# Kernel tuning notes

Measured on AMD Instinct MI355X. Metric: run time of the kernel, lower is better.

Reference implementation:

```python
import jax, jax.numpy as jnp
from jax import lax
import numpy as np

N, C, T, V = 128, 64, 128, 25   # batch, channels, frames, joints
S, R, O, K = 3, 8, 64, 5        # subsets, rel_channels, out_channels, temporal kernel
BC, AC = 16, 16                 # branch channels, attention channels
EPS = 1e-5


def _bn(x, g, b):
    # eval-mode BatchNorm2d with running_mean=0, running_var=1
    return x * (g / jnp.sqrt(1.0 + EPS))[None, :, None, None] + b[None, :, None, None]


def _c1x1(x, w, b):
    # 1x1 conv over channel dim; x [N,C,T,V], w [O,C], b [O]
    return jnp.einsum('oc,nctv->notv', w, x) + b[None, :, None, None]


def _tconv(x, w, b, d):
    # temporal conv, kernel (K,1), dilation (d,1), 'same' padding in T; w [O,I,K]
    pad = (K + (K - 1) * (d - 1) - 1) // 2
    out = lax.conv_general_dilated(x, w[..., None], (1, 1), [(pad, pad), (0, 0)],
                                   rhs_dilation=(d, 1),
                                   dimension_numbers=('NCHW', 'OIHW', 'NCHW'))
    return out + b[None, :, None, None]


def setup_inputs() -> dict:
    ks = iter(jax.random.split(jax.random.key(0), 40))
    nrm = lambda sh, s=0.1: jax.random.normal(next(ks), sh, jnp.float32) * s
    z = lambda sh: jnp.zeros(sh, jnp.float32)
    o = lambda sh: jnp.ones(sh, jnp.float32)
    return {
        'x': jax.random.normal(next(ks), (N, C, T, V), jnp.float32),
        'PA': nrm((S, V, V)),
        'alpha': o((S,)),
        'c1w': nrm((S, R, C)), 'c1b': z((S, R)),
        'c2w': nrm((S, R, C)), 'c2b': z((S, R)),
        'c3w': nrm((S, O, C)), 'c3b': z((S, O)),
        'c4w': nrm((S, O, R)), 'c4b': z((S, O)),
        'gbn_g': o((O,)), 'gbn_b': z((O,)),
        'att1_w': nrm((AC, O)), 'att1_b': z((AC,)),
        'att2_w': nrm((O, AC)), 'att2_b': z((O,)),
        'br_pw': nrm((2, BC, O)), 'br_pb': z((2, BC)),
        'br_pg': o((2, BC)), 'br_pbeta': z((2, BC)),
        'br_tw': nrm((2, BC, BC, K)), 'br_tb': z((2, BC)),
        'br_tg': o((2, BC)), 'br_tbeta': z((2, BC)),
        'mp_pw': nrm((BC, O)), 'mp_pb': z((BC,)),
        'mp_g1': o((BC,)), 'mp_b1': z((BC,)),
        'mp_g2': o((BC,)), 'mp_b2': z((BC,)),
        'p3w': nrm((BC, O)), 'p3b': z((BC,)),
        'p3g': o((BC,)), 'p3beta': z((BC,)),
    }


def reference(x, PA, alpha, c1w, c1b, c2w, c2b, c3w, c3b, c4w, c4b,
              gbn_g, gbn_b, att1_w, att1_b, att2_w, att2_b,
              br_pw, br_pb, br_pg, br_pbeta, br_tw, br_tb, br_tg, br_tbeta,
              mp_pw, mp_pb, mp_g1, mp_b1, mp_g2, mp_b2, p3w, p3b, p3g, p3beta):
    # ---- unit_ctrgcn: 3 CTRGC subsets vectorized over axis s ----
    xm = x.mean(axis=2)                                       # [N,C,V]; 1x1 conv commutes with mean over T
    x1 = jnp.einsum('src,ncv->nsrv', c1w, xm) + c1b[None, :, :, None]
    x2 = jnp.einsum('src,ncv->nsrv', c2w, xm) + c2b[None, :, :, None]
    x3 = jnp.einsum('soc,nctv->nsotv', c3w, x) + c3b[None, :, :, None, None]
    diff = jnp.tanh(x1[..., :, None] - x2[..., None, :])      # [N,S,R,U,V]
    aff = jnp.einsum('sor,nsruv->nsouv', c4w, diff) + c4b[None, :, :, None, None]
    Asym = PA + jnp.swapaxes(PA, -1, -2)                      # A + A^T, [S,V,V]
    aff = aff * alpha[None, :, None, None, None] + Asym[None, :, None, :, :]
    aff = jax.nn.softmax(aff, axis=-2)                        # softmax over u (dim=-2)
    y = jnp.einsum('nsouv,nsotv->notu', aff, x3)              # aggregate + sum over subsets
    y = _bn(y, gbn_g, gbn_b)
    # squeeze-excite channel attention
    pooled = y.mean(axis=(2, 3))                              # [N,O]
    h = jax.nn.relu(pooled @ att1_w.T + att1_b)
    se = jax.nn.sigmoid(h @ att2_w.T + att2_b)
    y = jax.nn.relu(y * se[:, :, None, None] + x)             # down = identity (in==out, stride 1)
    # ---- MultiScale_TemporalConv (residual=False), stride 1 ----
    outs = []
    for i, d in enumerate((1, 2)):
        p = jax.nn.relu(_bn(_c1x1(y, br_pw[i], br_pb[i]), br_pg[i], br_pbeta[i]))
        t = _tconv(p, br_tw[i], br_tb[i], d)
        outs.append(_bn(t, br_tg[i], br_tbeta[i]))
    p = jax.nn.relu(_bn(_c1x1(y, mp_pw, mp_pb), mp_g1, mp_b1))
    m = lax.reduce_window(p, -jnp.inf, lax.max, (1, 1, 3, 1), (1, 1, 1, 1),
                          [(0, 0), (0, 0), (1, 1), (0, 0)])   # MaxPool2d((3,1), stride 1, pad (1,0))
    outs.append(_bn(m, mp_g2, mp_b2))
    outs.append(_bn(_c1x1(y, p3w, p3b), p3g, p3beta))
    out = jnp.concatenate(outs, axis=1)
    return jax.nn.relu(out + x)                               # outer residual (identity) + relu
```

## Files before the change

kernel.cpp:

```cpp
#include <hip/hip_runtime.h>
#include <hip/hip_bf16.h>
#include <math.h>

#define N_  128
#define C_  64
#define T_  128
#define V_  25
#define S_  3
#define R_  8
#define O_  64
#define BC_ 16
#define TV_ 3200

typedef __attribute__((ext_vector_type(8))) short bf16x8;
typedef __attribute__((ext_vector_type(4))) float f32x4;

__device__ inline short f2bf(float f) {
  union { float f; unsigned u; } c; c.f = f;
  unsigned r = (c.u + 0x7FFFu + ((c.u >> 16) & 1u)) >> 16;
  return (short)r;
}
__device__ inline float bf2f(short s) {
  union { float f; unsigned u; } c; c.u = ((unsigned)(unsigned short)s) << 16;
  return c.f;
}

__global__ __launch_bounds__(256) void k_cvt(const float* __restrict__ x,
                                             const float* __restrict__ c3w,
                                             const float* __restrict__ br_tw,
                                             short* __restrict__ xbfT,
                                             short* __restrict__ c3wbf,
                                             short* __restrict__ w2g) {
  int bid = blockIdx.x;
  int tid = threadIdx.x;
  if (bid < 6400) {
    int n = bid / 50, pg = bid % 50;
    int w = tid >> 6, l = tid & 63;
    int p0 = pg * 64 + w * 16;
    const float* xp = x + ((size_t)n * 64 + l) * TV_ + p0;
    short* ob = xbfT + ((size_t)n * TV_ + p0) * 64 + l;
    #pragma unroll
    for (int q = 0; q < 4; ++q) {
      float4 xv = *(const float4*)(xp + q * 4);
      ob[(q * 4 + 0) * 64] = f2bf(xv.x);
      ob[(q * 4 + 1) * 64] = f2bf(xv.y);
      ob[(q * 4 + 2) * 64] = f2bf(xv.z);
      ob[(q * 4 + 3) * 64] = f2bf(xv.w);
    }
    if (bid < 144) {
      int i = bid * 256 + tid;
      c3wbf[i] = f2bf(c3w[i]);
    }
  } else {
    for (int i = tid; i < 6144; i += 256) {
      int plane = i / 3072, rem = i % 3072;
      int h = rem / 1536, rem2 = rem % 1536;
      int bc = rem2 / 96, kidx = rem2 % 96;
      short outv = 0;
      if (kidx < 80) {
        int ktap = kidx >> 4, ic = kidx & 15;
        float wv = br_tw[((h * 16 + bc) * 16 + ic) * 5 + ktap];
        short wb = f2bf(wv);
        outv = (plane == 0) ? wb : f2bf(wv - bf2f(wb));
      }
      w2g[i] = outv;
    }
  }
}

__global__ __launch_bounds__(256) void k_xm(const float* __restrict__ x,
                                            float* __restrict__ xm) {
  int nc = blockIdx.x;
  const float* xp = x + (size_t)nc * TV_;
  __shared__ float part[250];
  int tid = threadIdx.x;
  if (tid < 250) {
    float s = 0.f;
    for (int k = 0; k < 13; ++k) {
      int idx = tid + 250 * k;
      if (idx < TV_) s += xp[idx];
    }
    part[tid] = s;
  }
  __syncthreads();
  if (tid < 25) {
    float s = 0.f;
    #pragma unroll
    for (int g = 0; g < 10; ++g) s += part[g * 25 + tid];
    xm[(size_t)nc * V_ + tid] = s * (1.0f / 128.0f);
  }
}

__global__ __launch_bounds__(256) void k_aff(
    const float* __restrict__ xm, const float* __restrict__ PA,
    const float* __restrict__ alpha,
    const float* __restrict__ c1w, const float* __restrict__ c1b,
    const float* __restrict__ c2w, const float* __restrict__ c2b,
    const float* __restrict__ c4w, const float* __restrict__ c4b,
    short* __restrict__ affbf) {
  int oq = blockIdx.x, s = blockIdx.y, n = blockIdx.z;
  int tid = threadIdx.x;
  __shared__ float xml[1600];
  __shared__ float w1[512], w2[512], w4l[512];
  __shared__ float x1l[200], x2l[200];
  __shared__ float dift[625 * 9];
  __shared__ float asym[625];
  short* ab = affbf + (((size_t)n * S_ + s) * 64) * 1024;
  {
    int4 zz; zz.x = 0; zz.y = 0; zz.z = 0; zz.w = 0;
    int4* z0 = (int4*)(ab + (size_t)(oq * 8) * 1024);
    int4* z1 = (int4*)(ab + (size_t)(oq * 8 + 32) * 1024);
    for (int i = tid; i < 1024; i += 256) { z0[i] = zz; z1[i] = zz; }
  }
  for (int i = tid; i < 1600; i += 256) xml[i] = xm[(size_t)n * 1600 + i];
  for (int i = tid; i < 512; i += 256) {
    w1[i] = c1w[s * 512 + i];
    w2[i] = c2w[s * 512 + i];
    w4l[i] = c4w[s * 512 + i];
  }
  for (int i = tid; i < 625; i += 256) {
    int u = i / 25, v = i % 25;
    asym[i] = PA[s * 625 + u * 25 + v] + PA[s * 625 + v * 25 + u];
  }
  __syncthreads();
  if (tid < 200) {
    int r = tid / 25, v = tid % 25;
    float a1 = c1b[s * R_ + r], a2 = c2b[s * R_ + r];
    #pragma unroll
    for (int c = 0; c < 64; ++c) {
      float xv = xml[c * 25 + v];
      a1 = fmaf(w1[r * 64 + c], xv, a1);
      a2 = fmaf(w2[r * 64 + c], xv, a2);
    }
    x1l[tid] = a1; x2l[tid] = a2;
  }
  __syncthreads();
  for (int i = tid; i < 5000; i += 256) {
    int r = i / 625, rem = i % 625, u = rem / 25, v = rem % 25;
    dift[(u * 25 + v) * 9 + r] = tanhf(x1l[r * 25 + u] - x2l[r * 25 + v]);
  }
  __syncthreads();
  float al = alpha[s];
  if (tid < 200) {
    int ol = tid / 25, v = tid % 25;
    int oA = oq * 8 + ol, oB = oA + 32;
    float avA[25], avB[25];
    float bA = c4b[s * O_ + oA], bB = c4b[s * O_ + oB];
    #pragma unroll
    for (int u = 0; u < 25; ++u) { avA[u] = bA; avB[u] = bB; }
    #pragma unroll
    for (int u = 0; u < 25; ++u) {
      const float* dp = &dift[(u * 25 + v) * 9];
      #pragma unroll
      for (int r = 0; r < 8; ++r) {
        float d = dp[r];
        avA[u] = fmaf(w4l[oA * 8 + r], d, avA[u]);
        avB[u] = fmaf(w4l[oB * 8 + r], d, avB[u]);
      }
    }
    float mA = -1e30f, mB = -1e30f;
    #pragma unroll
    for (int u = 0; u < 25; ++u) {
      float as_ = asym[u * 25 + v];
      avA[u] = fmaf(avA[u], al, as_);
      avB[u] = fmaf(avB[u], al, as_);
      mA = fmaxf(mA, avA[u]); mB = fmaxf(mB, avB[u]);
    }
    float sA = 0.f, sB = 0.f;
    #pragma unroll
    for (int u = 0; u < 25; ++u) {
      avA[u] = expf(avA[u] - mA); sA += avA[u];
      avB[u] = expf(avB[u] - mB); sB += avB[u];
    }
    float iA = 1.0f / sA, iB = 1.0f / sB;
    #pragma unroll
    for (int u = 0; u < 25; ++u) {
      ab[(size_t)oA * 1024 + u * 32 + v] = f2bf(avA[u] * iA);
      ab[(size_t)oB * 1024 + u * 32 + v] = f2bf(avB[u] * iB);
    }
  }
}

__global__ __launch_bounds__(256) void k_gemm1(
    const short* __restrict__ xbfT, const short* __restrict__ c3wbf,
    const float* __restrict__ c3b, short* __restrict__ x3p, int n0) {
  int pt = blockIdx.x;
  int nn = blockIdx.y;
  int n = n0 + nn;
  int tid = threadIdx.x, w = tid >> 6, l = tid & 63;
  int lr = l & 15, lg = l >> 4;
  const short* xb = xbfT + ((size_t)n * TV_ + pt * 64) * 64;
  bf16x8 B[4][2];
  #pragma unroll
  for (int sub = 0; sub < 4; ++sub) {
    const short* rp = xb + (sub * 16 + lr) * 64 + lg * 8;
    B[sub][0] = *(const bf16x8*)(rp);
    B[sub][1] = *(const bf16x8*)(rp + 32);
  }
  bf16x8 A[3][2];
  #pragma unroll
  for (int m = 0; m < 3; ++m) {
    const short* rp = c3wbf + (size_t)((w * 3 + m) * 16 + lr) * 64 + lg * 8;
    A[m][0] = *(const bf16x8*)(rp);
    A[m][1] = *(const bf16x8*)(rp + 32);
  }
  f32x4 acc[3][4];
  #pragma unroll
  for (int m = 0; m < 3; ++m)
    #pragma unroll
    for (int sub = 0; sub < 4; ++sub) acc[m][sub] = (f32x4)(0.f);
  #pragma unroll
  for (int m = 0; m < 3; ++m)
    #pragma unroll
    for (int sub = 0; sub < 4; ++sub) {
      acc[m][sub] = __builtin_amdgcn_mfma_f32_16x16x32_bf16(A[m][0], B[sub][0], acc[m][sub], 0, 0, 0);
      acc[m][sub] = __builtin_amdgcn_mfma_f32_16x16x32_bf16(A[m][1], B[sub][1], acc[m][sub], 0, 0, 0);
    }
  int tl[4], vl[4];
  #pragma unroll
  for (int sub = 0; sub < 4; ++sub) {
    int pos = pt * 64 + sub * 16 + lr;
    tl[sub] = pos / 25; vl[sub] = pos - tl[sub] * 25;
  }
  #pragma unroll
  for (int m = 0; m < 3; ++m) {
    int mt = w * 3 + m;
    #pragma unroll
    for (int j = 0; j < 4; ++j) {
      int r = mt * 16 + lg * 4 + j;
      float bias = c3b[r];
      short* orow = x3p + (((size_t)nn * 192 + r) * 128) * 32;
      #pragma unroll
      for (int sub = 0; sub < 4; ++sub) {
        orow[tl[sub] * 32 + vl[sub]] = f2bf(acc[m][sub][j] + bias);
      }
    }
  }
}

__global__ __launch_bounds__(256) void k_gemm2(
    const short* __restrict__ x3p, const short* __restrict__ affbf,
    const float* __restrict__ gbn_g, const float* __restrict__ gbn_b,
    short* __restrict__ ybn, float* __restrict__ pooled, int n0) {
  int og = blockIdx.x;
  int nn = blockIdx.y;
  int n = n0 + nn;
  int tid = threadIdx.x, w = tid >> 6, l = tid & 63;
  int lr = l & 15, lg = l >> 4;
  int o = og * 4 + w;
  f32x4 acc[8][2];
  #pragma unroll
  for (int mt = 0; mt < 8; ++mt) { acc[mt][0] = (f32x4)(0.f); acc[mt][1] = (f32x4)(0.f); }
  const short* xb = x3p + (((size_t)nn * 3) * 64 + o) * 4096;
  const short* ab = affbf + (((size_t)n * 3) * 64 + o) * 1024;
  #pragma unroll
  for (int s = 0; s < 3; ++s) {
    const short* abs_ = ab + (size_t)s * 64 * 1024;
    bf16x8 Bf[2];
    Bf[0] = *(const bf16x8*)(abs_ + (0 * 16 + lr) * 32 + lg * 8);
    Bf[1] = *(const bf16x8*)(abs_ + (1 * 16 + lr) * 32 + lg * 8);
    const short* xbs = xb + (size_t)s * 64 * 4096;
    #pragma unroll
    for (int mt = 0; mt < 8; ++mt) {
      bf16x8 Af = *(const bf16x8*)(xbs + (mt * 16 + lr) * 32 + lg * 8);
      acc[mt][0] = __builtin_amdgcn_mfma_f32_16x16x32_bf16(Af, Bf[0], acc[mt][0], 0, 0, 0);
      acc[mt][1] = __builtin_amdgcn_mfma_f32_16x16x32_bf16(Af, Bf[1], acc[mt][1], 0, 0, 0);
    }
  }
  float rs = 1.0f / sqrtf(1.0f + 1e-5f);
  float sc = gbn_g[o] * rs, bb = gbn_b[o];
  short* yb = ybn + ((size_t)n * 64 + o) * TV_;
  float lsum = 0.f;
  #pragma unroll
  for (int mt = 0; mt < 8; ++mt) {
    #pragma unroll
    for (int j = 0; j < 4; ++j) {
      int t = mt * 16 + lg * 4 + j;
      float v0 = fmaf(acc[mt][0][j], sc, bb);
      yb[t * 25 + lr] = f2bf(v0); lsum += v0;
      if (lr < 9) {
        float v1 = fmaf(acc[mt][1][j], sc, bb);
        yb[t * 25 + 16 + lr] = f2bf(v1); lsum += v1;
      }
    }
  }
  #pragma unroll
  for (int off = 32; off > 0; off >>= 1) lsum += __shfl_down(lsum, off);
  if (l == 0) pooled[(size_t)n * 64 + o] = lsum;
}

__global__ __launch_bounds__(64) void k_se(
    const float* __restrict__ pooled,
    const float* __restrict__ att1_w, const float* __restrict__ att1_b,
    const float* __restrict__ att2_w, const float* __restrict__ att2_b,
    float* __restrict__ se) {
  int n = blockIdx.x; int tid = threadIdx.x;
  __shared__ float pl[64]; __shared__ float hbuf[16];
  pl[tid] = pooled[(size_t)n * 64 + tid] * (1.0f / 3200.0f);
  __syncthreads();
  if (tid < 16) {
    float a = att1_b[tid];
    #pragma unroll
    for (int o = 0; o < 64; ++o) a = fmaf(att1_w[tid * 64 + o], pl[o], a);
    hbuf[tid] = fmaxf(a, 0.f);
  }
  __syncthreads();
  float a2 = att2_b[tid];
  #pragma unroll
  for (int k = 0; k < 16; ++k) a2 = fmaf(att2_w[tid * 16 + k], hbuf[k], a2);
  se[(size_t)n * 64 + tid] = 1.0f / (1.0f + expf(-a2));
}

__global__ __launch_bounds__(256) void k_pw(
    const short* __restrict__ ybn, const float* __restrict__ se,
    const float* __restrict__ x,
    const float* __restrict__ br_pw, const float* __restrict__ br_pb,
    const float* __restrict__ br_pg, const float* __restrict__ br_pbeta,
    const float* __restrict__ mp_pw, const float* __restrict__ mp_pb,
    const float* __restrict__ mp_g1, const float* __restrict__ mp_b1,
    const float* __restrict__ p3w, const float* __restrict__ p3b,
    const float* __restrict__ p3g, const float* __restrict__ p3beta,
    short* __restrict__ pbuf, float* __restrict__ outp) {
  int tt = blockIdx.x; int n = blockIdx.y;
  int t0 = tt * 10;
  int npos = min(10, T_ - t0) * 25;
  int tid = threadIdx.x;
  if (tid >= npos) return;
  float rs = 1.0f / sqrtf(1.0f + 1e-5f);
  size_t base = (size_t)n * C_ * TV_ + (size_t)t0 * 25 + tid;
  int pos = t0 * 25 + tid;
  const float* sep = se + (size_t)n * 64;
  float y2[64]; float xhi[16];
  #pragma unroll
  for (int o = 0; o < 64; ++o) {
    float xv = x[base + (size_t)o * TV_];
    float yv = bf2f(ybn[base + (size_t)o * TV_]);
    y2[o] = fmaxf(fmaf(yv, sep[o], xv), 0.f);
    if (o >= 48) xhi[o - 48] = xv;
  }
  #pragma unroll
  for (int h = 0; h < 3; ++h) {
    const float* wp = (h == 0) ? br_pw : (h == 1) ? (br_pw + 1024) : mp_pw;
    short* po = pbuf + ((size_t)(h * N_ + n) * TV_ + pos) * 16;
    bf16x8 v0, v1;
    #pragma unroll
    for (int bc = 0; bc < 16; ++bc) {
      float g, beta, pb;
      if (h < 2) { g = br_pg[h * 16 + bc]; beta = br_pbeta[h * 16 + bc]; pb = br_pb[h * 16 + bc]; }
      else       { g = mp_g1[bc];          beta = mp_b1[bc];             pb = mp_pb[bc]; }
      float a = 0.f;
      #pragma unroll
      for (int o = 0; o < 64; ++o) a = fmaf(wp[bc * 64 + o], y2[o], a);
      short pk = f2bf(fmaxf(fmaf(a + pb, g * rs, beta), 0.f));
      if (bc < 8) v0[bc] = pk; else v1[bc - 8] = pk;
    }
    *(bf16x8*)(po) = v0;
    *(bf16x8*)(po + 8) = v1;
  }
  #pragma unroll
  for (int bc = 0; bc < 16; ++bc) {
    float a = 0.f;
    #pragma unroll
    for (int o = 0; o < 64; ++o) a = fmaf(p3w[bc * 64 + o], y2[o], a);
    float ov = fmaf(a + p3b[bc], p3g[bc] * rs, p3beta[bc]);
    outp[base + (size_t)(48 + bc) * TV_] = fmaxf(ov + xhi[bc], 0.f);
  }
}

__global__ __launch_bounds__(256) void k_tcm(
    const short* __restrict__ pbuf, const short* __restrict__ w2g,
    const float* __restrict__ x,
    const float* __restrict__ br_tb, const float* __restrict__ br_tg,
    const float* __restrict__ br_tbeta,
    float* __restrict__ outp) {
  int tt = blockIdx.x, h = blockIdx.y, n = blockIdx.z;
  int d = 1 + h;
  int tid = threadIdx.x, w = tid >> 6, l = tid & 63;
  int lr = l & 15, lg = l >> 4;
  __shared__ short ptile[72 * 25 * 16];
  {
    const int4* src = (const int4*)(pbuf + ((size_t)(h * N_ + n) * TV_) * 16);
    int4* dst = (int4*)ptile;
    int4 zz; zz.x = 0; zz.y = 0; zz.z = 0; zz.w = 0;
    for (int u = tid; u < 3600; u += 256) {
      int r = u / 50, q = u - r * 50;
      int t = tt * 64 - 4 + r;
      dst[u] = (t >= 0 && t < T_) ? src[t * 50 + q] : zz;
    }
  }
  bf16x8 Af0[3], Af1[3];
  #pragma unroll
  for (int ks = 0; ks < 3; ++ks) {
    Af0[ks] = *(const bf16x8*)(w2g + ((0 * 2 + h) * 16 + lr) * 96 + ks * 32 + lg * 8);
    Af1[ks] = *(const bf16x8*)(w2g + ((1 * 2 + h) * 16 + lr) * 96 + ks * 32 + lg * 8);
  }
  float rs = 1.0f / sqrtf(1.0f + 1e-5f);
  float scl[4], shf[4];
  #pragma unroll
  for (int j = 0; j < 4; ++j) {
    int bc = lg * 4 + j;
    float sc = br_tg[h * 16 + bc] * rs;
    scl[j] = sc;
    shf[j] = fmaf(br_tb[h * 16 + bc], sc, br_tbeta[h * 16 + bc]);
  }
  __syncthreads();
  for (int nt = w; nt < 100; nt += 4) {
    int posL = nt * 16 + lr;
    int tL = posL / 25, v = posL - tL * 25;
    f32x4 acc = (f32x4)(0.f);
    #pragma unroll
    for (int ks = 0; ks < 3; ++ks) {
      int ktap = 2 * ks + (lg >> 1);
      int ic0 = (lg & 1) * 8;
      int r = tL + 4 + (ktap - 2) * d;
      r = min(r, 71);
      bf16x8 Bf = *(const bf16x8*)(ptile + (r * 25 + v) * 16 + ic0);
      acc = __builtin_amdgcn_mfma_f32_16x16x32_bf16(Af0[ks], Bf, acc, 0, 0, 0);
      acc = __builtin_amdgcn_mfma_f32_16x16x32_bf16(Af1[ks], Bf, acc, 0, 0, 0);
    }
    int gpos = tt * 1600 + posL;
    #pragma unroll
    for (int j = 0; j < 4; ++j) {
      int ch = h * 16 + lg * 4 + j;
      size_t oa = ((size_t)n * 64 + ch) * TV_ + gpos;
      float xv = x[oa];
      outp[oa] = fmaxf(fmaf(acc[j], scl[j], shf[j]) + xv, 0.f);
    }
  }
}

__global__ __launch_bounds__(256) void k_mp(
    const short* __restrict__ pbuf, const float* __restrict__ x,
    const float* __restrict__ mp_g2, const float* __restrict__ mp_b2,
    float* __restrict__ outp) {
  int tt = blockIdx.x, n = blockIdx.y;
  int t0 = tt * 10;
  int npos = min(10, T_ - t0) * 25;
  int tid = threadIdx.x;
  if (tid >= npos) return;
  int pos = t0 * 25 + tid;
  int t = pos / 25, v = pos - t * 25;
  const short* pb = pbuf + ((size_t)(2 * N_ + n) * TV_) * 16;
  int tm = max(t - 1, 0), tp = min(t + 1, T_ - 1);
  bf16x8 a0 = *(const bf16x8*)(pb + (tm * 25 + v) * 16);
  bf16x8 a1 = *(const bf16x8*)(pb + (tm * 25 + v) * 16 + 8);
  bf16x8 b0 = *(const bf16x8*)(pb + (t  * 25 + v) * 16);
  bf16x8 b1 = *(const bf16x8*)(pb + (t  * 25 + v) * 16 + 8);
  bf16x8 c0 = *(const bf16x8*)(pb + (tp * 25 + v) * 16);
  bf16x8 c1 = *(const bf16x8*)(pb + (tp * 25 + v) * 16 + 8);
  float rs = 1.0f / sqrtf(1.0f + 1e-5f);
  #pragma unroll
  for (int i = 0; i < 8; ++i) {
    float m0 = fmaxf(fmaxf(bf2f(a0[i]), bf2f(b0[i])), bf2f(c0[i]));
    float m1 = fmaxf(fmaxf(bf2f(a1[i]), bf2f(b1[i])), bf2f(c1[i]));
    size_t oa0 = ((size_t)n * 64 + 32 + i) * TV_ + pos;
    size_t oa1 = ((size_t)n * 64 + 40 + i) * TV_ + pos;
    float v0 = fmaf(m0, mp_g2[i] * rs, mp_b2[i]);
    float v1 = fmaf(m1, mp_g2[8 + i] * rs, mp_b2[8 + i]);
    outp[oa0] = fmaxf(v0 + x[oa0], 0.f);
    outp[oa1] = fmaxf(v1 + x[oa1], 0.f);
  }
}

extern "C" void kernel_launch(void* const* d_in, const int* in_sizes, int n_in,
                              void* d_out, int out_size, void* d_ws, size_t ws_size,
                              hipStream_t stream) {
  (void)in_sizes; (void)n_in; (void)out_size; (void)ws_size;
  const float* x      = (const float*)d_in[0];
  const float* PA     = (const float*)d_in[1];
  const float* alpha  = (const float*)d_in[2];
  const float* c1w    = (const float*)d_in[3];
  const float* c1b    = (const float*)d_in[4];
  const float* c2w    = (const float*)d_in[5];
  const float* c2b    = (const float*)d_in[6];
  const float* c3w    = (const float*)d_in[7];
  const float* c3b    = (const float*)d_in[8];
  const float* c4w    = (const float*)d_in[9];
  const float* c4b    = (const float*)d_in[10];
  const float* gbn_g  = (const float*)d_in[11];
  const float* gbn_b  = (const float*)d_in[12];
  const float* att1_w = (const float*)d_in[13];
  const float* att1_b = (const float*)d_in[14];
  const float* att2_w = (const float*)d_in[15];
  const float* att2_b = (const float*)d_in[16];
  const float* br_pw  = (const float*)d_in[17];
  const float* br_pb  = (const float*)d_in[18];
  const float* br_pg  = (const float*)d_in[19];
  const float* br_pbeta = (const float*)d_in[20];
  const float* br_tw  = (const float*)d_in[21];
  const float* br_tb  = (const float*)d_in[22];
  const float* br_tg  = (const float*)d_in[23];
  const float* br_tbeta = (const float*)d_in[24];
  const float* mp_pw  = (const float*)d_in[25];
  const float* mp_pb  = (const float*)d_in[26];
  const float* mp_g1  = (const float*)d_in[27];
  const float* mp_b1  = (const float*)d_in[28];
  const float* mp_g2  = (const float*)d_in[29];
  const float* mp_b2  = (const float*)d_in[30];
  const float* p3w    = (const float*)d_in[31];
  const float* p3b    = (const float*)d_in[32];
  const float* p3g    = (const float*)d_in[33];
  const float* p3beta = (const float*)d_in[34];
  float* out = (float*)d_out;
  float* ws  = (float*)d_ws;

  float* xm_b    = ws;
  float* pooled  = ws + 204800;
  float* se_b    = ws + 212992;
  short* xbfT    = (short*)(ws + 221184);
  short* affbf   = (short*)(ws + 13328384);
  short* x3p     = (short*)(ws + 25911296);
  short* ybn     = (short*)(ws + 38494208);
  short* c3wbf   = (short*)(ws + 51601408);
  short* w2g     = (short*)(ws + 51619840);
  short* p_b     = (short*)(ws + 13328384);

  k_cvt<<<dim3(6401),        dim3(256), 0, stream>>>(x, c3w, br_tw, xbfT, c3wbf, w2g);
  k_xm <<<dim3(N_ * C_),     dim3(256), 0, stream>>>(x, xm_b);
  k_aff<<<dim3(4, 3, N_),    dim3(256), 0, stream>>>(xm_b, PA, alpha, c1w, c1b, c2w, c2b,
                                                     c4w, c4b, affbf);
  for (int ch = 0; ch < 4; ++ch) {
    k_gemm1<<<dim3(50, 32), dim3(256), 0, stream>>>(xbfT, c3wbf, c3b, x3p, ch * 32);
    k_gemm2<<<dim3(16, 32), dim3(256), 0, stream>>>(x3p, affbf, gbn_g, gbn_b, ybn, pooled, ch * 32);
  }
  k_se <<<dim3(N_),          dim3(64),  0, stream>>>(pooled, att1_w, att1_b, att2_w, att2_b, se_b);
  k_pw <<<dim3(13, N_),      dim3(256), 0, stream>>>(ybn, se_b, x, br_pw, br_pb, br_pg, br_pbeta,
                                                     mp_pw, mp_pb, mp_g1, mp_b1,
                                                     p3w, p3b, p3g, p3beta, p_b, out);
  k_tcm<<<dim3(2, 2, N_),    dim3(256), 0, stream>>>(p_b, w2g, x, br_tb, br_tg, br_tbeta, out);
  k_mp <<<dim3(13, N_),      dim3(256), 0, stream>>>(p_b, x, mp_g2, mp_b2, out);
}
```

Measured before the change: 671.3 us.

## Move pointwise branch convolutions onto MFMA with split-bf16 weights and folded BN

Replaces the scalar-FMA pointwise kernel, which held 64 y2 values per thread, with an MFMA kernel. Each block stages a 128-position tile of y2 as hi/lo bf16 pairs in swizzled LDS, and each wave computes one 16-channel branch through three bf16 MFMAs to approximate fp32 accuracy. BN scale and bias are folded into precomputed split-bf16 weights and a shift vector inside the conversion kernel. This removes heavy per-thread FMA work and register pressure, at the cost of extra LDS traffic and a small approximation error.

```diff
diff --git a/kernel.cpp b/kernel.cpp
--- a/kernel.cpp
+++ b/kernel.cpp
@@ -28,11 +28,26 @@
 __global__ __launch_bounds__(256) void k_cvt(const float* __restrict__ x,
                                              const float* __restrict__ c3w,
                                              const float* __restrict__ br_tw,
+                                             const float* __restrict__ br_pw,
+                                             const float* __restrict__ br_pb,
+                                             const float* __restrict__ br_pg,
+                                             const float* __restrict__ br_pbeta,
+                                             const float* __restrict__ mp_pw,
+                                             const float* __restrict__ mp_pb,
+                                             const float* __restrict__ mp_g1,
+                                             const float* __restrict__ mp_b1,
+                                             const float* __restrict__ p3w,
+                                             const float* __restrict__ p3b,
+                                             const float* __restrict__ p3g,
+                                             const float* __restrict__ p3beta,
                                              short* __restrict__ xbfT,
                                              short* __restrict__ c3wbf,
-                                             short* __restrict__ w2g) {
+                                             short* __restrict__ w2g,
+                                             short* __restrict__ wcbf,
+                                             float* __restrict__ wcsh) {
   int bid = blockIdx.x;
   int tid = threadIdx.x;
+  float rs = 1.0f / sqrtf(1.0f + 1e-5f);
   if (bid < 6400) {
     int n = bid / 50, pg = bid % 50;
     int w = tid >> 6, l = tid & 63;
@@ -64,6 +79,27 @@
         outv = (plane == 0) ? wb : f2bf(wv - bf2f(wb));
       }
       w2g[i] = outv;
+    }
+    for (int i = tid; i < 4096; i += 256) {
+      int r = i / 64, c = i % 64;
+      int br = r >> 4, bc = r & 15;
+      float wv, g;
+      if (br < 2)      { wv = br_pw[br * 1024 + bc * 64 + c]; g = br_pg[br * 16 + bc]; }
+      else if (br == 2){ wv = mp_pw[bc * 64 + c];             g = mp_g1[bc]; }
+      else             { wv = p3w[bc * 64 + c];               g = p3g[bc]; }
+      float ws_ = wv * (g * rs);
+      short hi = f2bf(ws_);
+      wcbf[i] = hi;
+      wcbf[4096 + i] = f2bf(ws_ - bf2f(hi));
+    }
+    if (tid < 64) {
+      int r = tid;
+      int br = r >> 4, bc = r & 15;
+      float g, pb, beta;
+      if (br < 2)      { g = br_pg[br * 16 + bc]; pb = br_pb[br * 16 + bc]; beta = br_pbeta[br * 16 + bc]; }
+      else if (br == 2){ g = mp_g1[bc];           pb = mp_pb[bc];           beta = mp_b1[bc]; }
+      else             { g = p3g[bc];             pb = p3b[bc];             beta = p3beta[bc]; }
+      wcsh[r] = fmaf(pb, g * rs, beta);
     }
   }
 }
@@ -311,59 +347,84 @@
   se[(size_t)n * 64 + tid] = 1.0f / (1.0f + expf(-a2));
 }
 
-__global__ __launch_bounds__(256) void k_pw(
+__global__ __launch_bounds__(256) void k_pwm(
     const short* __restrict__ ybn, const float* __restrict__ se,
     const float* __restrict__ x,
-    const float* __restrict__ br_pw, const float* __restrict__ br_pb,
-    const float* __restrict__ br_pg, const float* __restrict__ br_pbeta,
-    const float* __restrict__ mp_pw, const float* __restrict__ mp_pb,
-    const float* __restrict__ mp_g1, const float* __restrict__ mp_b1,
-    const float* __restrict__ p3w, const float* __restrict__ p3b,
-    const float* __restrict__ p3g, const float* __restrict__ p3beta,
+    const short* __restrict__ wcbf, const float* __restrict__ wcsh,
     short* __restrict__ pbuf, float* __restrict__ outp) {
-  int tt = blockIdx.x; int n = blockIdx.y;
-  int t0 = tt * 10;
-  int npos = min(10, T_ - t0) * 25;
+  int pt = blockIdx.x; int n = blockIdx.y;
   int tid = threadIdx.x;
-  if (tid >= npos) return;
-  float rs = 1.0f / sqrtf(1.0f + 1e-5f);
-  size_t base = (size_t)n * C_ * TV_ + (size_t)t0 * 25 + tid;
-  int pos = t0 * 25 + tid;
-  const float* sep = se + (size_t)n * 64;
-  float y2[64]; float xhi[16];
-  #pragma unroll
-  for (int o = 0; o < 64; ++o) {
-    float xv = x[base + (size_t)o * TV_];
-    float yv = bf2f(ybn[base + (size_t)o * TV_]);
-    y2[o] = fmaxf(fmaf(yv, sep[o], xv), 0.f);
-    if (o >= 48) xhi[o - 48] = xv;
-  }
-  #pragma unroll
-  for (int h = 0; h < 3; ++h) {
-    const float* wp = (h == 0) ? br_pw : (h == 1) ? (br_pw + 1024) : mp_pw;
-    short* po = pbuf + ((size_t)(h * N_ + n) * TV_ + pos) * 16;
-    bf16x8 v0, v1;
-    #pragma unroll
-    for (int bc = 0; bc < 16; ++bc) {
-      float g, beta, pb;
-      if (h < 2) { g = br_pg[h * 16 + bc]; beta = br_pbeta[h * 16 + bc]; pb = br_pb[h * 16 + bc]; }
-      else       { g = mp_g1[bc];          beta = mp_b1[bc];             pb = mp_pb[bc]; }
-      float a = 0.f;
+  __shared__ short yl[2][128 * 64];
+  {
+    int posL = tid & 127, ch = tid >> 7;
+    int pos0 = pt * 128;
+    const float* sep = se + (size_t)n * 64;
+    float y2r[32];
+    #pragma unroll
+    for (int i = 0; i < 32; ++i) {
+      int c = ch * 32 + i;
+      size_t a = ((size_t)n * 64 + c) * TV_ + pos0 + posL;
+      float xv = x[a];
+      float yv = bf2f(ybn[a]);
+      y2r[i] = fmaxf(fmaf(yv, sep[c], xv), 0.f);
+    }
+    #pragma unroll
+    for (int q = 0; q < 4; ++q) {
+      bf16x8 hi, lo;
       #pragma unroll
-      for (int o = 0; o < 64; ++o) a = fmaf(wp[bc * 64 + o], y2[o], a);
-      short pk = f2bf(fmaxf(fmaf(a + pb, g * rs, beta), 0.f));
-      if (bc < 8) v0[bc] = pk; else v1[bc - 8] = pk;
-    }
-    *(bf16x8*)(po) = v0;
-    *(bf16x8*)(po + 8) = v1;
-  }
-  #pragma unroll
-  for (int bc = 0; bc < 16; ++bc) {
-    float a = 0.f;
-    #pragma unroll
-    for (int o = 0; o < 64; ++o) a = fmaf(p3w[bc * 64 + o], y2[o], a);
-    float ov = fmaf(a + p3b[bc], p3g[bc] * rs, p3beta[bc]);
-    outp[base + (size_t)(48 + bc) * TV_] = fmaxf(ov + xhi[bc], 0.f);
+      for (int j = 0; j < 8; ++j) {
+        float v = y2r[q * 8 + j];
+        short hb = f2bf(v);
+        hi[j] = hb;
+        lo[j] = f2bf(v - bf2f(hb));
+      }
+      int cc = ch * 4 + q;
+      int ccs = cc ^ (posL & 7);
+      *(bf16x8*)&yl[0][posL * 64 + ccs * 8] = hi;
+      *(bf16x8*)&yl[1][posL * 64 + ccs * 8] = lo;
+    }
+  }
+  __syncthreads();
+  int w = tid >> 6, l = tid & 63;
+  int lr = l & 15, lg = l >> 4;
+  bf16x8 A0[2], A1[2];
+  #pragma unroll
+  for (int kk = 0; kk < 2; ++kk) {
+    A0[kk] = *(const bf16x8*)(wcbf +        (w * 16 + lr) * 64 + kk * 32 + lg * 8);
+    A1[kk] = *(const bf16x8*)(wcbf + 4096 + (w * 16 + lr) * 64 + kk * 32 + lg * 8);
+  }
+  float shf[4];
+  #pragma unroll
+  for (int j = 0; j < 4; ++j) shf[j] = wcsh[w * 16 + lg * 4 + j];
+  #pragma unroll
+  for (int nt = 0; nt < 8; ++nt) {
+    int posL = nt * 16 + lr;
+    f32x4 acc = (f32x4)(0.f);
+    #pragma unroll
+    for (int kk = 0; kk < 2; ++kk) {
+      int ccs = (kk * 4 + lg) ^ (posL & 7);
+      bf16x8 B0 = *(const bf16x8*)&yl[0][posL * 64 + ccs * 8];
+      bf16x8 B1 = *(const bf16x8*)&yl[1][posL * 64 + ccs * 8];
+      acc = __builtin_amdgcn_mfma_f32_16x16x32_bf16(A0[kk], B0, acc, 0, 0, 0);
+      acc = __builtin_amdgcn_mfma_f32_16x16x32_bf16(A0[kk], B1, acc, 0, 0, 0);
+      acc = __builtin_amdgcn_mfma_f32_16x16x32_bf16(A1[kk], B0, acc, 0, 0, 0);
+    }
+    int pos = pt * 128 + posL;
+    if (w < 3) {
+      short4 pk;
+      pk.x = f2bf(fmaxf(acc[0] + shf[0], 0.f));
+      pk.y = f2bf(fmaxf(acc[1] + shf[1], 0.f));
+      pk.z = f2bf(fmaxf(acc[2] + shf[2], 0.f));
+      pk.w = f2bf(fmaxf(acc[3] + shf[3], 0.f));
+      *(short4*)&pbuf[(((size_t)w * N_ + n) * TV_ + pos) * 16 + lg * 4] = pk;
+    } else {
+      #pragma unroll
+      for (int j = 0; j < 4; ++j) {
+        int ch8 = 48 + lg * 4 + j;
+        size_t oa = ((size_t)n * 64 + ch8) * TV_ + pos;
+        outp[oa] = fmaxf(acc[j] + shf[j] + x[oa], 0.f);
+      }
+    }
   }
 }
 
@@ -513,9 +574,15 @@
   short* ybn     = (short*)(ws + 38494208);
   short* c3wbf   = (short*)(ws + 51601408);
   short* w2g     = (short*)(ws + 51619840);
+  short* wcbf    = (short*)(ws + 51622912);
+  float* wcsh    = ws + 51627008;
   short* p_b     = (short*)(ws + 13328384);
 
-  k_cvt<<<dim3(6401),        dim3(256), 0, stream>>>(x, c3w, br_tw, xbfT, c3wbf, w2g);
+  k_cvt<<<dim3(6401),        dim3(256), 0, stream>>>(x, c3w, br_tw,
+                                                     br_pw, br_pb, br_pg, br_pbeta,
+                                                     mp_pw, mp_pb, mp_g1, mp_b1,
+                                                     p3w, p3b, p3g, p3beta,
+                                                     xbfT, c3wbf, w2g, wcbf, wcsh);
   k_xm <<<dim3(N_ * C_),     dim3(256), 0, stream>>>(x, xm_b);
   k_aff<<<dim3(4, 3, N_),    dim3(256), 0, stream>>>(xm_b, PA, alpha, c1w, c1b, c2w, c2b,
                                                      c4w, c4b, affbf);
@@ -524,9 +591,7 @@
     k_gemm2<<<dim3(16, 32), dim3(256), 0, stream>>>(x3p, affbf, gbn_g, gbn_b, ybn, pooled, ch * 32);
   }
   k_se <<<dim3(N_),          dim3(64),  0, stream>>>(pooled, att1_w, att1_b, att2_w, att2_b, se_b);
-  k_pw <<<dim3(13, N_),      dim3(256), 0, stream>>>(ybn, se_b, x, br_pw, br_pb, br_pg, br_pbeta,
-                                                     mp_pw, mp_pb, mp_g1, mp_b1,
-                                                     p3w, p3b, p3g, p3beta, p_b, out);
+  k_pwm<<<dim3(25, N_),      dim3(256), 0, stream>>>(ybn, se_b, x, wcbf, wcsh, p_b, out);
   k_tcm<<<dim3(2, 2, N_),    dim3(256), 0, stream>>>(p_b, w2g, x, br_tb, br_tg, br_tbeta, out);
   k_mp <<<dim3(13, N_),      dim3(256), 0, stream>>>(p_b, x, mp_g2, mp_b2, out);
 }
```

Measured after the change: 653.9 us. 2.6% less time.
